# Optimization experiments

Measured on AMD Instinct MI355X. Metric: run time of the kernel, lower is better.

The kernel has to match this reference:

```python
import jax, jax.numpy as jnp
import numpy as np

H = 8  # number of heads


def setup_inputs() -> dict:
    key = jax.random.key(0)
    ks = jax.random.split(key, 7)
    B, L, D = 4, 2048, 512
    dh = D // H
    s = 1.0 / np.sqrt(D).astype(np.float32)
    return {
        "q": jax.random.normal(ks[0], (B, L, D), jnp.float32),
        "k": jax.random.normal(ks[1], (B, L, D), jnp.float32),
        "v": jax.random.normal(ks[2], (B, L, D), jnp.float32),
        "Wq": jax.random.normal(ks[3], (D, D), jnp.float32) * s,
        "Wk": jax.random.normal(ks[4], (D, D), jnp.float32) * s,
        "Wv": jax.random.normal(ks[5], (D, D), jnp.float32) * s,
        "E": jax.random.normal(ks[6], (L, dh), jnp.float32) * s,
    }


def _skew(QE):
    # QE: [B, H, L, L] -> pad one column on the left, reshape to [B,H,L+1,L],
    # drop the first row: the classic Music Transformer skewing trick.
    B, h, L, M = QE.shape
    padded = jnp.pad(QE, ((0, 0), (0, 0), (0, 0), (1, 0)))
    return padded.reshape(B, h, M + 1, L)[:, :, 1:, :]


def reference(q, k, v, Wq, Wk, Wv, E):
    B, L, D = q.shape
    dh = D // H

    def heads(x, W):
        return jnp.einsum('bld,de->ble', x, W).reshape(B, L, H, dh).transpose(0, 2, 1, 3)

    qh = heads(q, Wq)  # [B,H,L,dh]
    kh = heads(k, Wk)
    vh = heads(v, Wv)

    QE = jnp.einsum('bhld,md->bhlm', qh, E)      # [B,H,L,L]
    Srel = _skew(QE)                             # [B,H,L,L]
    QKt = jnp.einsum('bhld,bhmd->bhlm', qh, kh)  # [B,H,L,L]

    # NOTE: original divides AFTER softmax (faithful to source).
    attn = jax.nn.softmax(QKt + Srel, axis=-1) / float(np.sqrt(dh))
    out = jnp.einsum('bhlm,bhmd->bhld', attn, vh)
    return out.transpose(0, 2, 1, 3).reshape(B, L, D)
```

## Files before the change

### kernel.cpp

```cpp
#include <hip/hip_runtime.h>
#include <hip/hip_bf16.h>
#include <math.h>

typedef _Float16 f16;
typedef __attribute__((ext_vector_type(8))) _Float16 f16x8;
typedef __attribute__((ext_vector_type(4))) _Float16 f16x4;
typedef __attribute__((ext_vector_type(4))) float f32x4;

namespace {
constexpr int B = 4, L = 2048, D = 512, NH = 8, DH = 64;
}

__global__ __launch_bounds__(256)
void ecast_kernel(const float* __restrict__ E, f16* __restrict__ Ef) {
    int i4 = (blockIdx.x * 256 + threadIdx.x) * 4;
    float4 x = *(const float4*)(E + i4);
    *(f16x4*)(Ef + i4) = (f16x4){(f16)x.x, (f16)x.y, (f16)x.z, (f16)x.w};
}

__global__ __launch_bounds__(256)
void wtrans_kernel(const float* __restrict__ Wq, const float* __restrict__ Wk,
                   const float* __restrict__ Wv, f16* __restrict__ Wt) {
    __shared__ f16 Ws[64 * 65];
    const int sel = blockIdx.z;
    const float* W = (sel == 0) ? Wq : (sel == 1) ? Wk : Wv;
    f16* Wo = Wt + (size_t)sel * D * D;
    const int k0 = blockIdx.x * 64, n0 = blockIdx.y * 64;
    const int t = threadIdx.x;
#pragma unroll
    for (int i = 0; i < 16; ++i) {
        int idx = 256 * i + t;
        int r = idx >> 6, c = idx & 63;
        Ws[r * 65 + c] = (f16)W[(size_t)(k0 + r) * D + n0 + c];
    }
    __syncthreads();
    const int c = t >> 2, kseg = t & 3;
    f16x8 r0, r1;
#pragma unroll
    for (int j = 0; j < 8; ++j) r0[j] = Ws[(kseg * 16 + j) * 65 + c];
#pragma unroll
    for (int j = 0; j < 8; ++j) r1[j] = Ws[(kseg * 16 + 8 + j) * 65 + c];
    f16* o = Wo + (size_t)(n0 + c) * D + k0 + kseg * 16;
    *(f16x8*)o = r0;
    *(f16x8*)(o + 8) = r1;
}

__global__ __launch_bounds__(256, 4)
void proj_gemm(const float* __restrict__ q, const float* __restrict__ k,
               const float* __restrict__ v, const f16* __restrict__ Wt,
               f16* __restrict__ Qf, f16* __restrict__ Kf, f16* __restrict__ Vtf) {
    __shared__ f16 As[128 * 72];
    __shared__ f16 Bs[64 * 72];
    const int bx = blockIdx.x, by = blockIdx.y;
    const int sel = by >> 3, h = by & 7;
    const int m0 = bx * 128;
    const float* X = (sel == 0) ? q : (sel == 1) ? k : v;
    const f16* Bt = Wt + (size_t)sel * D * D + (size_t)h * 64 * D;
    const int t = threadIdx.x, wid = t >> 6, lane = t & 63;
    const int quad = lane >> 4, col = lane & 15;
    const int mw = wid * 32;

    f32x4 acc[2][4];
#pragma unroll
    for (int i = 0; i < 2; ++i)
#pragma unroll
        for (int j = 0; j < 4; ++j) acc[i][j] = (f32x4){0.f, 0.f, 0.f, 0.f};

    float4 xa[8];
    f16x8 breg[2];
    auto loadG = [&](int k0) {
#pragma unroll
        for (int i = 0; i < 8; ++i) {
            int idx = 256 * i + t;
            int r = idx >> 4, c4 = idx & 15;
            xa[i] = *(const float4*)(X + (size_t)(m0 + r) * D + k0 + c4 * 4);
        }
#pragma unroll
        for (int i = 0; i < 2; ++i) {
            int idx = 256 * i + t;
            int r = idx >> 3, ch = idx & 7;
            breg[i] = *(const f16x8*)(Bt + (size_t)r * D + k0 + ch * 8);
        }
    };
    auto storeL = [&]() {
#pragma unroll
        for (int i = 0; i < 8; ++i) {
            int idx = 256 * i + t;
            int r = idx >> 4, c4 = idx & 15;
            *(f16x4*)(As + r * 72 + c4 * 4) =
                (f16x4){(f16)xa[i].x, (f16)xa[i].y, (f16)xa[i].z, (f16)xa[i].w};
        }
#pragma unroll
        for (int i = 0; i < 2; ++i) {
            int idx = 256 * i + t;
            int r = idx >> 3, ch = idx & 7;
            *(f16x8*)(Bs + r * 72 + ch * 8) = breg[i];
        }
    };

    loadG(0);
    for (int k0 = 0; k0 < D; k0 += 64) {
        __syncthreads();
        storeL();
        __syncthreads();
        if (k0 + 64 < D) loadG(k0 + 64);
#pragma unroll
        for (int ks = 0; ks < 2; ++ks) {
            f16x8 af[2], bf[4];
#pragma unroll
            for (int mt = 0; mt < 2; ++mt)
                af[mt] = *(const f16x8*)(As + (mw + mt * 16 + col) * 72 + quad * 8 + ks * 32);
#pragma unroll
            for (int nt = 0; nt < 4; ++nt)
                bf[nt] = *(const f16x8*)(Bs + (nt * 16 + col) * 72 + quad * 8 + ks * 32);
#pragma unroll
            for (int mt = 0; mt < 2; ++mt)
#pragma unroll
                for (int nt = 0; nt < 4; ++nt)
                    acc[mt][nt] = __builtin_amdgcn_mfma_f32_16x16x32_f16(af[mt], bf[nt], acc[mt][nt], 0, 0, 0);
        }
    }

    if (sel < 2) {
        f16* Y = (sel == 0) ? Qf : Kf;
#pragma unroll
        for (int mt = 0; mt < 2; ++mt)
#pragma unroll
            for (int nt = 0; nt < 4; ++nt)
#pragma unroll
                for (int reg = 0; reg < 4; ++reg) {
                    int m = m0 + mw + mt * 16 + quad * 4 + reg;
                    int bb = m >> 11, l = m & 2047, d = nt * 16 + col;
                    Y[((size_t)(bb * NH + h) * L + l) * DH + d] = (f16)acc[mt][nt][reg];
                }
    } else {
        __syncthreads();
        f16* Cs = As;
#pragma unroll
        for (int mt = 0; mt < 2; ++mt)
#pragma unroll
            for (int nt = 0; nt < 4; ++nt)
#pragma unroll
                for (int reg = 0; reg < 4; ++reg) {
                    int d = nt * 16 + col;
                    int lc = mw + mt * 16 + quad * 4 + reg;
                    Cs[d * 136 + lc] = (f16)acc[mt][nt][reg];
                }
        __syncthreads();
        const int dd = t >> 2, seg = t & 3;
        const int bb = m0 >> 11, l0 = m0 & 2047;
        f16* Yv = Vtf + ((size_t)(bb * NH + h) * DH + dd) * L + l0 + seg * 32;
#pragma unroll
        for (int j = 0; j < 4; ++j)
            *(f16x8*)(Yv + j * 8) = *(const f16x8*)(Cs + dd * 136 + seg * 32 + j * 8);
    }
}

__global__ __launch_bounds__(256, 4)
void attn_kernel(const f16* __restrict__ Qf, const f16* __restrict__ Kf,
                 const f16* __restrict__ Vtf, const f16* __restrict__ Ef,
                 float* __restrict__ out) {
    __shared__ f16 KfS[64 * 72];
    __shared__ f16 VfS[64 * 72];
    __shared__ f16 Pbuf[4][16 * 72];

    const int t = threadIdx.x, wid = t >> 6, lane = t & 63;
    const int quad = lane >> 4, col = lane & 15;
    const int l0w = blockIdx.x * 64 + wid * 16;
    const int h = blockIdx.y, bb = blockIdx.z;
    const size_t head = (size_t)(bb * NH + h) * (size_t)(L * DH);
    const f16* qf = Qf + head;
    const f16* kf = Kf + head;
    const f16* vt = Vtf + head;
    f16* Pw = Pbuf[wid];

    f16x8 qF[2], qS[2];
    {
        const int m = l0w + col;
        const int mS = min(m + 1, L - 1);
#pragma unroll
        for (int ks = 0; ks < 2; ++ks) {
            const int off = quad * 8 + ks * 32;
            qF[ks] = *(const f16x8*)(qf + (size_t)m * DH + off);
            qS[ks] = *(const f16x8*)(qf + (size_t)mS * DH + off);
        }
    }

    f16x8 kreg[2], vreg[2];
    auto loadKV = [&](int c0) {
#pragma unroll
        for (int i = 0; i < 2; ++i) {
            int idx = 256 * i + t;
            int r = idx >> 3, ch = idx & 7;
            kreg[i] = *(const f16x8*)(kf + (size_t)(c0 + r) * DH + ch * 8);
            vreg[i] = *(const f16x8*)(vt + (size_t)r * L + c0 + ch * 8);
        }
    };

    f32x4 O[4];
#pragma unroll
    for (int i = 0; i < 4; ++i) O[i] = (f32x4){0.f, 0.f, 0.f, 0.f};
    float mrow[4] = {-1e30f, -1e30f, -1e30f, -1e30f};
    float srow[4] = {0.f, 0.f, 0.f, 0.f};

    loadKV(0);
    for (int c0 = 0; c0 < L; c0 += 64) {
        __syncthreads();
#pragma unroll
        for (int i = 0; i < 2; ++i) {
            int idx = 256 * i + t;
            int r = idx >> 3, ch = idx & 7;
            *(f16x8*)(KfS + r * 72 + ch * 8) = kreg[i];
            *(f16x8*)(VfS + r * 72 + ch * 8) = vreg[i];
        }
        __syncthreads();
        if (c0 + 64 < L) loadKV(c0 + 64);

        const int d0 = c0 - l0w;

        f32x4 S[4];
#pragma unroll
        for (int ns = 0; ns < 4; ++ns) {
            S[ns] = (f32x4){0.f, 0.f, 0.f, 0.f};
#pragma unroll
            for (int ks = 0; ks < 2; ++ks) {
                f16x8 bh = *(const f16x8*)(KfS + (ns * 16 + col) * 72 + quad * 8 + ks * 32);
                S[ns] = __builtin_amdgcn_mfma_f32_16x16x32_f16(qF[ks], bh, S[ns], 0, 0, 0);
            }
        }

        const bool doA = (d0 <= 15);
        const bool doB = (d0 >= -61);
#pragma unroll 1
        for (int pass = 0; pass < 2; ++pass) {
            if ((pass == 0 && !doA) || (pass == 1 && !doB)) continue;
            const int jbase = (pass == 0) ? (d0 + L - 16) : (d0 - 17);
            f32x4 G[5];
#pragma unroll
            for (int g = 0; g < 5; ++g) {
                int er = min(max(jbase + g * 16 + col, 0), L - 1);
                G[g] = (f32x4){0.f, 0.f, 0.f, 0.f};
                const size_t eb = (size_t)er * DH + quad * 8;
#pragma unroll
                for (int ks = 0; ks < 2; ++ks) {
                    f16x8 e8 = *(const f16x8*)(Ef + eb + ks * 32);
                    G[g] = __builtin_amdgcn_mfma_f32_16x16x32_f16(
                               (pass == 0) ? qF[ks] : qS[ks], e8, G[g], 0, 0, 0);
                }
            }
#pragma unroll
            for (int reg = 0; reg < 4; ++reg) {
                const int r  = quad * 4 + reg;
                const int jj = col - r + 15;
                const int src = quad * 16 + (jj & 15);
#pragma unroll
                for (int ns = 0; ns < 4; ++ns) {
                    float v0 = __shfl(G[ns][reg], src, 64);
                    float v1 = __shfl(G[ns + 1][reg], src, 64);
                    float val = (jj < 16) ? v0 : v1;
                    const int rel = d0 + ns * 16 + col - r;
                    const bool use = (pass == 0) ? (rel <= 0) : (rel >= 2);
                    if (use) S[ns][reg] += val;
                }
            }
        }

#pragma unroll
        for (int reg = 0; reg < 4; ++reg) {
            float tm = fmaxf(fmaxf(S[0][reg], S[1][reg]), fmaxf(S[2][reg], S[3][reg]));
#pragma unroll
            for (int msk = 1; msk < 16; msk <<= 1)
                tm = fmaxf(tm, __shfl_xor(tm, msk, 16));
            const float mnew  = fmaxf(mrow[reg], tm);
            const float alpha = __expf(mrow[reg] - mnew);
            float p[4], ps = 0.f;
#pragma unroll
            for (int ns = 0; ns < 4; ++ns) { p[ns] = __expf(S[ns][reg] - mnew); ps += p[ns]; }
#pragma unroll
            for (int msk = 1; msk < 16; msk <<= 1)
                ps += __shfl_xor(ps, msk, 16);
            srow[reg] = srow[reg] * alpha + ps;
            mrow[reg] = mnew;
            const int r = quad * 4 + reg;
#pragma unroll
            for (int ns = 0; ns < 4; ++ns) {
                O[ns][reg] *= alpha;
                Pw[r * 72 + ns * 16 + col] = (f16)p[ns];
            }
        }

        f16x8 pA[2];
        pA[0] = *(const f16x8*)(Pw + col * 72 + quad * 8);
        pA[1] = *(const f16x8*)(Pw + col * 72 + 32 + quad * 8);
#pragma unroll
        for (int ns = 0; ns < 4; ++ns) {
#pragma unroll
            for (int ks = 0; ks < 2; ++ks) {
                f16x8 v8 = *(const f16x8*)(VfS + (ns * 16 + col) * 72 + quad * 8 + ks * 32);
                O[ns] = __builtin_amdgcn_mfma_f32_16x16x32_f16(pA[ks], v8, O[ns], 0, 0, 0);
            }
        }
    }

#pragma unroll
    for (int reg = 0; reg < 4; ++reg) {
        const int l = l0w + quad * 4 + reg;
        const float inv = 1.0f / (srow[reg] * 8.0f);
        float* o = out + ((size_t)bb * L + l) * D + h * DH;
#pragma unroll
        for (int ns = 0; ns < 4; ++ns)
            o[ns * 16 + col] = O[ns][reg] * inv;
    }
}

extern "C" void kernel_launch(void* const* d_in, const int* in_sizes, int n_in,
                              void* d_out, int out_size, void* d_ws, size_t ws_size,
                              hipStream_t stream) {
    const float* q  = (const float*)d_in[0];
    const float* k  = (const float*)d_in[1];
    const float* v  = (const float*)d_in[2];
    const float* Wq = (const float*)d_in[3];
    const float* Wk = (const float*)d_in[4];
    const float* Wv = (const float*)d_in[5];
    const float* E  = (const float*)d_in[6];
    float* out = (float*)d_out;

    const size_t plane = (size_t)B * NH * L * DH;
    f16* Qf  = (f16*)d_ws;
    f16* Kfp = Qf + plane;
    f16* Vtf = Kfp + plane;
    f16* Wt  = Vtf + plane;
    f16* Ef  = Wt + (size_t)3 * D * D;

    ecast_kernel<<<L * DH / 1024, 256, 0, stream>>>(E, Ef);
    wtrans_kernel<<<dim3(8, 8, 3), 256, 0, stream>>>(Wq, Wk, Wv, Wt);
    proj_gemm<<<dim3(64, 24), 256, 0, stream>>>(q, k, v, Wt, Qf, Kfp, Vtf);
    attn_kernel<<<dim3(L / 64, NH, B), 256, 0, stream>>>(Qf, Kfp, Vtf, Ef, out);
}
```

Measured before the change: 352.6 us.

## Pre-cast inputs to fp16, prefetch E rows, and single-shuffle skew gather

After: 787.7 us. 123% more time.

```diff
diff --git a/kernel.cpp b/kernel.cpp
--- a/kernel.cpp
+++ b/kernel.cpp
@@ -9,6 +9,20 @@
 
 namespace {
 constexpr int B = 4, L = 2048, D = 512, NH = 8, DH = 64;
+constexpr int M = B * L;
+}
+
+__global__ __launch_bounds__(256)
+void xcast_kernel(const float* __restrict__ q, const float* __restrict__ k,
+                  const float* __restrict__ v, f16* __restrict__ X) {
+    const int sel = blockIdx.y;
+    const float* src = (sel == 0) ? q : (sel == 1) ? k : v;
+    size_t i8 = ((size_t)blockIdx.x * 256 + threadIdx.x) * 8;
+    float4 a = *(const float4*)(src + i8);
+    float4 b = *(const float4*)(src + i8 + 4);
+    f16x8 o = {(f16)a.x, (f16)a.y, (f16)a.z, (f16)a.w,
+               (f16)b.x, (f16)b.y, (f16)b.z, (f16)b.w};
+    *(f16x8*)(X + (size_t)sel * M * D + i8) = o;
 }
 
 __global__ __launch_bounds__(256)
@@ -46,15 +60,14 @@
 }
 
 __global__ __launch_bounds__(256, 4)
-void proj_gemm(const float* __restrict__ q, const float* __restrict__ k,
-               const float* __restrict__ v, const f16* __restrict__ Wt,
+void proj_gemm(const f16* __restrict__ X, const f16* __restrict__ Wt,
                f16* __restrict__ Qf, f16* __restrict__ Kf, f16* __restrict__ Vtf) {
     __shared__ f16 As[128 * 72];
     __shared__ f16 Bs[64 * 72];
     const int bx = blockIdx.x, by = blockIdx.y;
     const int sel = by >> 3, h = by & 7;
     const int m0 = bx * 128;
-    const float* X = (sel == 0) ? q : (sel == 1) ? k : v;
+    const f16* Xp = X + (size_t)sel * M * D;
     const f16* Bt = Wt + (size_t)sel * D * D + (size_t)h * 64 * D;
     const int t = threadIdx.x, wid = t >> 6, lane = t & 63;
     const int quad = lane >> 4, col = lane & 15;
@@ -66,14 +79,13 @@
 #pragma unroll
         for (int j = 0; j < 4; ++j) acc[i][j] = (f32x4){0.f, 0.f, 0.f, 0.f};
 
-    float4 xa[8];
-    f16x8 breg[2];
+    f16x8 xa16[4], breg[2];
     auto loadG = [&](int k0) {
 #pragma unroll
-        for (int i = 0; i < 8; ++i) {
-            int idx = 256 * i + t;
-            int r = idx >> 4, c4 = idx & 15;
-            xa[i] = *(const float4*)(X + (size_t)(m0 + r) * D + k0 + c4 * 4);
+        for (int i = 0; i < 4; ++i) {
+            int idx = 256 * i + t;
+            int r = idx >> 3, ch = idx & 7;
+            xa16[i] = *(const f16x8*)(Xp + (size_t)(m0 + r) * D + k0 + ch * 8);
         }
 #pragma unroll
         for (int i = 0; i < 2; ++i) {
@@ -84,11 +96,10 @@
     };
     auto storeL = [&]() {
 #pragma unroll
-        for (int i = 0; i < 8; ++i) {
-            int idx = 256 * i + t;
-            int r = idx >> 4, c4 = idx & 15;
-            *(f16x4*)(As + r * 72 + c4 * 4) =
-                (f16x4){(f16)xa[i].x, (f16)xa[i].y, (f16)xa[i].z, (f16)xa[i].w};
+        for (int i = 0; i < 4; ++i) {
+            int idx = 256 * i + t;
+            int r = idx >> 3, ch = idx & 7;
+            *(f16x8*)(As + r * 72 + ch * 8) = xa16[i];
         }
 #pragma unroll
         for (int i = 0; i < 2; ++i) {
@@ -106,18 +117,18 @@
         if (k0 + 64 < D) loadG(k0 + 64);
 #pragma unroll
         for (int ks = 0; ks < 2; ++ks) {
-            f16x8 af[2], bf[4];
+            f16x8 af[2], bfr[4];
 #pragma unroll
             for (int mt = 0; mt < 2; ++mt)
                 af[mt] = *(const f16x8*)(As + (mw + mt * 16 + col) * 72 + quad * 8 + ks * 32);
 #pragma unroll
             for (int nt = 0; nt < 4; ++nt)
-                bf[nt] = *(const f16x8*)(Bs + (nt * 16 + col) * 72 + quad * 8 + ks * 32);
+                bfr[nt] = *(const f16x8*)(Bs + (nt * 16 + col) * 72 + quad * 8 + ks * 32);
 #pragma unroll
             for (int mt = 0; mt < 2; ++mt)
 #pragma unroll
                 for (int nt = 0; nt < 4; ++nt)
-                    acc[mt][nt] = __builtin_amdgcn_mfma_f32_16x16x32_f16(af[mt], bf[nt], acc[mt][nt], 0, 0, 0);
+                    acc[mt][nt] = __builtin_amdgcn_mfma_f32_16x16x32_f16(af[mt], bfr[nt], acc[mt][nt], 0, 0, 0);
         }
     }
 
@@ -197,6 +208,19 @@
         }
     };
 
+    f16x8 eP[5][2];
+    auto prefetchE = [&](int d0n) {
+        const bool doAn = (d0n <= 15);
+        const int jbase0 = doAn ? (d0n + L - 16) : (d0n - 17);
+#pragma unroll
+        for (int g = 0; g < 5; ++g) {
+            int er = min(max(jbase0 + g * 16 + col, 0), L - 1);
+            const size_t eb = (size_t)er * DH + quad * 8;
+            eP[g][0] = *(const f16x8*)(Ef + eb);
+            eP[g][1] = *(const f16x8*)(Ef + eb + 32);
+        }
+    };
+
     f32x4 O[4];
 #pragma unroll
     for (int i = 0; i < 4; ++i) O[i] = (f32x4){0.f, 0.f, 0.f, 0.f};
@@ -204,6 +228,7 @@
     float srow[4] = {0.f, 0.f, 0.f, 0.f};
 
     loadKV(0);
+    prefetchE(0 - l0w);
     for (int c0 = 0; c0 < L; c0 += 64) {
         __syncthreads();
 #pragma unroll
@@ -234,36 +259,43 @@
 #pragma unroll 1
         for (int pass = 0; pass < 2; ++pass) {
             if ((pass == 0 && !doA) || (pass == 1 && !doB)) continue;
+            const bool pre = doA ? (pass == 0) : (pass == 1);
             const int jbase = (pass == 0) ? (d0 + L - 16) : (d0 - 17);
             f32x4 G[5];
 #pragma unroll
             for (int g = 0; g < 5; ++g) {
-                int er = min(max(jbase + g * 16 + col, 0), L - 1);
+                f16x8 e0, e1;
+                if (pre) {
+                    e0 = eP[g][0]; e1 = eP[g][1];
+                } else {
+                    int er = min(max(jbase + g * 16 + col, 0), L - 1);
+                    const size_t eb = (size_t)er * DH + quad * 8;
+                    e0 = *(const f16x8*)(Ef + eb);
+                    e1 = *(const f16x8*)(Ef + eb + 32);
+                }
                 G[g] = (f32x4){0.f, 0.f, 0.f, 0.f};
-                const size_t eb = (size_t)er * DH + quad * 8;
-#pragma unroll
-                for (int ks = 0; ks < 2; ++ks) {
-                    f16x8 e8 = *(const f16x8*)(Ef + eb + ks * 32);
-                    G[g] = __builtin_amdgcn_mfma_f32_16x16x32_f16(
-                               (pass == 0) ? qF[ks] : qS[ks], e8, G[g], 0, 0, 0);
-                }
+                G[g] = __builtin_amdgcn_mfma_f32_16x16x32_f16(
+                           (pass == 0) ? qF[0] : qS[0], e0, G[g], 0, 0, 0);
+                G[g] = __builtin_amdgcn_mfma_f32_16x16x32_f16(
+                           (pass == 0) ? qF[1] : qS[1], e1, G[g], 0, 0, 0);
             }
 #pragma unroll
             for (int reg = 0; reg < 4; ++reg) {
-                const int r  = quad * 4 + reg;
-                const int jj = col - r + 15;
-                const int src = quad * 16 + (jj & 15);
+                const int r = quad * 4 + reg;
+                const int src = quad * 16 + ((col - r + 15) & 15);
+                const bool hiG = (col >= 15 - r);
 #pragma unroll
                 for (int ns = 0; ns < 4; ++ns) {
-                    float v0 = __shfl(G[ns][reg], src, 64);
-                    float v1 = __shfl(G[ns + 1][reg], src, 64);
-                    float val = (jj < 16) ? v0 : v1;
+                    const float tmp = hiG ? G[ns][reg] : G[ns + 1][reg];
+                    const float val = __shfl(tmp, src, 64);
                     const int rel = d0 + ns * 16 + col - r;
                     const bool use = (pass == 0) ? (rel <= 0) : (rel >= 2);
                     if (use) S[ns][reg] += val;
                 }
             }
         }
+
+        if (c0 + 64 < L) prefetchE(d0 + 64);
 
 #pragma unroll
         for (int reg = 0; reg < 4; ++reg) {
@@ -331,9 +363,11 @@
     f16* Vtf = Kfp + plane;
     f16* Wt  = Vtf + plane;
     f16* Ef  = Wt + (size_t)3 * D * D;
-
+    f16* Xf  = Ef + (size_t)L * DH;
+
+    xcast_kernel<<<dim3((size_t)M * D / 2048, 3), 256, 0, stream>>>(q, k, v, Xf);
     ecast_kernel<<<L * DH / 1024, 256, 0, stream>>>(E, Ef);
     wtrans_kernel<<<dim3(8, 8, 3), 256, 0, stream>>>(Wq, Wk, Wv, Wt);
-    proj_gemm<<<dim3(64, 24), 256, 0, stream>>>(q, k, v, Wt, Qf, Kfp, Vtf);
+    proj_gemm<<<dim3(64, 24), 256, 0, stream>>>(Xf, Wt, Qf, Kfp, Vtf);
     attn_kernel<<<dim3(L / 64, NH, B), 256, 0, stream>>>(Qf, Kfp, Vtf, Ef, out);
 }
```
